# Optimization experiments

Hardware: AMD Instinct MI355X
Metric: run time of the kernel (lower is better)

## Reference

```python
import jax, jax.numpy as jnp
import numpy as np
from jax import lax

B = 4096; NLAG = 20; NT = 100; DIMH = 128; DIMPI = 2
DT = 0.01; MU1 = 0.06; MU2 = 0.02; R = 0.02; SIGMA = 0.2
BETA = 0.05; ETA = 0.5; LAMBD = 1.0; LOGEPS = 1e-6; UTIL_PENALTY = 100.0
FINAL_DISC = float(np.exp(-BETA * NT * DT))
Y_DECAY = float(np.exp(-DT * LAMBD))
# eqn.exp_array: discount weights for the lagged history (length n_lag)
EXP_ARRAY = np.exp(-LAMBD * DT * np.arange(NLAG, 0, -1)).astype(np.float32)
# eqn.geometric_sum: scalar weight on the oldest history point
GEOM = float((1.0 - np.exp(-LAMBD * DT)) / LAMBD * np.exp(-LAMBD * DT * NLAG))


def setup_inputs() -> dict:
    key = jax.random.key(0)
    ks = jax.random.split(key, 8)
    dw_sample = jax.random.normal(ks[0], (B, NT), jnp.float32) * np.sqrt(DT)
    x_init = jax.random.uniform(ks[1], (B, NLAG + 1), jnp.float32, 0.5, 1.5)
    s = 1.0 / np.sqrt(DIMH + 2)
    W_f = jax.random.normal(ks[2], (DIMH + 2, DIMH), jnp.float32) * s
    W_i = jax.random.normal(ks[3], (DIMH + 2, DIMH), jnp.float32) * s
    W_o = jax.random.normal(ks[4], (DIMH + 2, DIMH), jnp.float32) * s
    W_c = jax.random.normal(ks[5], (DIMH + 2, DIMH), jnp.float32) * s
    W_pi = jax.random.normal(ks[6], (DIMH, DIMPI), jnp.float32) * (1.0 / np.sqrt(DIMH))
    return {
        'dw_sample': dw_sample, 'x_init': x_init,
        'W_f': W_f, 'b_f': jnp.zeros((DIMH,), jnp.float32),
        'W_i': W_i, 'b_i': jnp.zeros((DIMH,), jnp.float32),
        'W_o': W_o, 'b_o': jnp.zeros((DIMH,), jnp.float32),
        'W_c': W_c, 'b_c': jnp.zeros((DIMH,), jnp.float32),
        'W_pi': W_pi, 'b_pi': jnp.zeros((DIMPI,), jnp.float32),
    }


def _forward(dw_sample, x_init, W_f, b_f, W_i, b_i, W_o, b_o, W_c, b_c, W_pi, b_pi):
    # Fuse the 4 gate Dense layers into one matmul (same math).
    W_all = jnp.concatenate([W_f, W_i, W_o, W_c], axis=1)   # [H+2, 4H]
    b_all = jnp.concatenate([b_f, b_i, b_o, b_c], axis=0)   # [4H]
    exp_arr = jnp.asarray(EXP_ARRAY)

    def cell(t_scal, x_col, h, C):
        tv = jnp.full((x_col.shape[0], 1), t_scal, x_col.dtype)
        z = jnp.concatenate([x_col, h, tv], axis=1)          # [B, H+2]
        g = z @ W_all + b_all                                # [B, 4H]
        f, i, o, cb = jnp.split(g, 4, axis=1)
        C = C * jax.nn.sigmoid(f) + jnp.tanh(cb) * jax.nn.sigmoid(i)
        h = jax.nn.sigmoid(o) * jnp.tanh(C)
        pi = h @ W_pi + b_pi                                 # [B, 2]
        return pi, h, C

    def util(v):
        return jnp.log(jax.nn.relu(v) + LOGEPS)

    # hidden_init (fixinit=False): warm up LSTM over n_lag history steps
    h0 = jnp.concatenate([x_init[:, 0:1], jnp.zeros((B, DIMH - 1), x_init.dtype)], axis=1)
    C0 = h0
    init_ts = jnp.arange(-NLAG, 0, dtype=x_init.dtype) * DT  # [NLAG]
    init_xs = x_init[:, 1:].T                                # [NLAG, B]

    def init_step(carry, inp):
        h, C = carry
        tval, xcol = inp
        _, h, C = cell(tval, xcol[:, None], h, C)
        return (h, C), None

    (h, C), _ = lax.scan(init_step, (h0, C0), (init_ts, init_xs))

    x = x_init[:, -1]
    y = jnp.sum(exp_arr * x_init[:, 1:], axis=-1) * DT + GEOM * x_init[:, 0]
    reward = jnp.zeros((B,), x.dtype)

    def step(carry, inp):
        x, y, h, C, reward = carry
        t_i, dw = inp
        t = t_i.astype(x.dtype)
        pi, h, C = cell(t * DT, x[:, None], h, C)
        pi = jax.nn.sigmoid(pi) * 2.0                        # final_pi_tf
        p0, p1 = pi[:, 0], pi[:, 1]
        inst_r = util(p0 * x) * jnp.exp(-BETA * t * DT) - jax.nn.relu(-x) * UTIL_PENALTY
        reward = reward + inst_r * DT
        dx = ((MU1 - R) * p1 - p0 + R) * x + MU2 * y
        x = x + dx * DT + SIGMA * x * p1 * dw
        y = y * Y_DECAY + x * DT
        return (x, y, h, C, reward), None

    ts = jnp.arange(NT)
    (x, y, h, C, reward), _ = lax.scan(step, (x, y, h, C, reward), (ts, dw_sample.T))

    # t == nt terminal step
    reward = reward + util(x + ETA * y) / BETA * FINAL_DISC - jax.nn.relu(-x) * UTIL_PENALTY
    return -reward


def reference(dw_sample, x_init, W_f, b_f, W_i, b_i, W_o, b_o, W_c, b_c, W_pi, b_pi):
    return _forward(dw_sample, x_init, W_f, b_f, W_i, b_i, W_o, b_o, W_c, b_c, W_pi, b_pi)
```

## Files before the change

### kernel.cpp

```cpp
#include <hip/hip_runtime.h>

#define NLAGC 20
#define NTC   100
#define DTC   0.01f
#define MU1C  0.06f
#define MU2C  0.02f
#define RC    0.02f
#define SIGC  0.2f
#define BETAC 0.05f
#define ETAC  0.5f
#define EPSC  1e-6f
#define UPENC 100.0f
#define YDECC 0.99004983374916805f
#define FDISCC 0.95122942450071403f
#define GEOMC 0.0081465072f
#define DFACTC 0.99950012497916927f

#define SPB 16
#define TPB 512
#define NKT 4
#define ZSTR 136

typedef __attribute__((ext_vector_type(8))) short short8v;
typedef __attribute__((ext_vector_type(4))) float f32x4;

__device__ __forceinline__ float sigm(float x){ return __builtin_amdgcn_rcpf(1.0f+__expf(-x)); }
__device__ __forceinline__ float tanhr(float x){ return 1.0f-2.0f*__builtin_amdgcn_rcpf(1.0f+__expf(2.0f*x)); }
__device__ __forceinline__ unsigned short f2bf(float f){
    unsigned u=__float_as_uint(f);
    u += 0x7fffu + ((u>>16)&1u);
    return (unsigned short)(u>>16);
}
__device__ __forceinline__ unsigned short f2bf_rna(float f){
    return (unsigned short)((__float_as_uint(f)+0x8000u)>>16);
}

__global__ __launch_bounds__(TPB,2) void polstm(
    const float* __restrict__ dw,  const float* __restrict__ xin,
    const float* __restrict__ Wf,  const float* __restrict__ bfp,
    const float* __restrict__ Wi,  const float* __restrict__ bip,
    const float* __restrict__ Wo,  const float* __restrict__ bop,
    const float* __restrict__ Wc,  const float* __restrict__ bcp,
    const float* __restrict__ Wpi, const float* __restrict__ bpi,
    float* __restrict__ out)
{
    __shared__ __align__(16) unsigned short zbuf[2][SPB*ZSTR];
    __shared__ float dwl[SPB*NTC];
    __shared__ float xl[SPB*21];
    __shared__ __align__(16) float pibuf[2][SPB];

    const int tid=threadIdx.x, w=tid>>6, lane=tid&63, col=lane&15, kg=lane>>4;
    const int j=w*16+col;
    const int base=blockIdx.x*SPB;

    for(int e=tid;e<2*SPB*ZSTR;e+=TPB) ((unsigned short*)zbuf)[e]=0;
    for(int e=tid;e<SPB*NTC;e+=TPB) dwl[e]=dw[base*NTC+e];
    for(int e=tid;e<SPB*21;e+=TPB)  xl[e]=xin[base*21+e];

    short8v bw[4][NKT], bpif[NKT];
    float wx[4], wt[4], bg[4];
    #pragma unroll
    for(int g=0;g<4;++g){
        const float* Wp=(g==0)?Wf:(g==1)?Wi:(g==2)?Wo:Wc;
        const float* bv=(g==0)?bfp:(g==1)?bip:(g==2)?bop:bcp;
        wx[g]=Wp[j]; wt[g]=Wp[129*128+j]; bg[g]=bv[j];
        #pragma unroll
        for(int kt=0;kt<NKT;++kt){
            short8v f;
            #pragma unroll
            for(int i=0;i<8;++i) f[i]=(short)f2bf(Wp[(1+kt*32+kg*8+i)*128+j]);
            bw[g][kt]=f;
        }
    }
    #pragma unroll
    for(int kt=0;kt<NKT;++kt){
        short8v f;
        #pragma unroll
        for(int i=0;i<8;++i){
            int k=kt*32+kg*8+i;
            int idx=k*2+((col<2)?col:0);
            float v=Wpi[idx];
            f[i]=(short)((col<2)?f2bf(v):(unsigned short)0);
        }
        bpif[kt]=f;
    }
    const float bp0=bpi[0], bp1=bpi[1];

    __syncthreads();

    float C[4];
    #pragma unroll
    for(int r=0;r<4;++r) C[r]=(j==0)?xl[(kg*4+r)*21]:0.0f;

    float xs=0.f, ys=0.f, rew=0.f;
    if(lane<SPB){
        float x0=xl[lane*21];
        xs=xl[lane*21+20];
        float acc=0.f;
        #pragma unroll
        for(int i=0;i<NLAGC;++i) acc+=__expf(-DTC*(float)(NLAGC-i))*xl[lane*21+1+i];
        ys=acc*DTC+GEOMC*x0;
    }
    if(j==0){
        #pragma unroll
        for(int r=0;r<4;++r) zbuf[0][(kg*4+r)*ZSTR+0]=f2bf(xl[(kg*4+r)*21]);
    }

    unsigned short* zr=zbuf[0];
    unsigned short* zw=zbuf[1];

    #pragma unroll 1
    for(int m=0;m<NLAGC;++m){
        __syncthreads();
        short8v av[NKT];
        {   const unsigned short* zp=zr+col*ZSTR+kg*8;
            #pragma unroll
            for(int kt=0;kt<NKT;++kt) av[kt]=*(const short8v*)(zp+kt*32);
        }
        float tval=(float)(m-NLAGC)*DTC;
        float xr0=xl[(kg*4+0)*21+1+m], xr1=xl[(kg*4+1)*21+1+m];
        float xr2=xl[(kg*4+2)*21+1+m], xr3=xl[(kg*4+3)*21+1+m];
        float b0=fmaf(wt[0],tval,bg[0]), b1=fmaf(wt[1],tval,bg[1]);
        float b2=fmaf(wt[2],tval,bg[2]), b3=fmaf(wt[3],tval,bg[3]);
        f32x4 a0={fmaf(wx[0],xr0,b0),fmaf(wx[0],xr1,b0),fmaf(wx[0],xr2,b0),fmaf(wx[0],xr3,b0)};
        f32x4 a1={fmaf(wx[1],xr0,b1),fmaf(wx[1],xr1,b1),fmaf(wx[1],xr2,b1),fmaf(wx[1],xr3,b1)};
        f32x4 a2={fmaf(wx[2],xr0,b2),fmaf(wx[2],xr1,b2),fmaf(wx[2],xr2,b2),fmaf(wx[2],xr3,b2)};
        f32x4 a3={fmaf(wx[3],xr0,b3),fmaf(wx[3],xr1,b3),fmaf(wx[3],xr2,b3),fmaf(wx[3],xr3,b3)};
        #pragma unroll
        for(int kt=0;kt<NKT;++kt){
            a0=__builtin_amdgcn_mfma_f32_16x16x32_bf16(av[kt],bw[0][kt],a0,0,0,0);
            a1=__builtin_amdgcn_mfma_f32_16x16x32_bf16(av[kt],bw[1][kt],a1,0,0,0);
            a2=__builtin_amdgcn_mfma_f32_16x16x32_bf16(av[kt],bw[2][kt],a2,0,0,0);
            a3=__builtin_amdgcn_mfma_f32_16x16x32_bf16(av[kt],bw[3][kt],a3,0,0,0);
        }
        #pragma unroll
        for(int r=0;r<4;++r){
            C[r]=C[r]*sigm(a0[r])+tanhr(a3[r])*sigm(a1[r]);
            float h=sigm(a2[r])*tanhr(C[r]);
            zw[(kg*4+r)*ZSTR+j]=f2bf_rna(h);
        }
        unsigned short* tp=zr; zr=zw; zw=tp;
    }

    float disc=1.0f;
    #pragma unroll 1
    for(int t=0;t<=NTC;++t){
        __syncthreads();
        short8v av[NKT];
        {   const unsigned short* zp=zr+col*ZSTR+kg*8;
            #pragma unroll
            for(int kt=0;kt<NKT;++kt) av[kt]=*(const short8v*)(zp+kt*32);
        }
        f32x4 a4={0.f,0.f,0.f,0.f};
        #pragma unroll
        for(int kt=0;kt<NKT;++kt)
            a4=__builtin_amdgcn_mfma_f32_16x16x32_bf16(av[kt],bpif[kt],a4,0,0,0);
        float tval=(float)t*DTC;
        float tb0=fmaf(wt[0],tval,bg[0]), tb1=fmaf(wt[1],tval,bg[1]);
        float tb2=fmaf(wt[2],tval,bg[2]), tb3=fmaf(wt[3],tval,bg[3]);
        f32x4 a0={tb0,tb0,tb0,tb0}, a1={tb1,tb1,tb1,tb1};
        f32x4 a2={tb2,tb2,tb2,tb2}, a3={tb3,tb3,tb3,tb3};
        #pragma unroll
        for(int kt=0;kt<NKT;++kt){
            a0=__builtin_amdgcn_mfma_f32_16x16x32_bf16(av[kt],bw[0][kt],a0,0,0,0);
            a1=__builtin_amdgcn_mfma_f32_16x16x32_bf16(av[kt],bw[1][kt],a1,0,0,0);
            a2=__builtin_amdgcn_mfma_f32_16x16x32_bf16(av[kt],bw[2][kt],a2,0,0,0);
            a3=__builtin_amdgcn_mfma_f32_16x16x32_bf16(av[kt],bw[3][kt],a3,0,0,0);
        }
        if(col<2) *(f32x4*)&pibuf[col][kg*4] = a4;
        if(t>0 && lane<SPB){
            float p0=2.0f*sigm(pibuf[0][lane]+bp0);
            float p1=2.0f*sigm(pibuf[1][lane]+bp1);
            float ir=__logf(fmaxf(p0*xs,0.f)+EPSC)*disc-fmaxf(-xs,0.f)*UPENC;
            rew+=ir*DTC;
            float dxv=((MU1C-RC)*p1-p0+RC)*xs+MU2C*ys;
            xs=xs+dxv*DTC+SIGC*xs*p1*dwl[lane*NTC+(t-1)];
            ys=ys*YDECC+xs*DTC;
        }
        if(t>0) disc*=DFACTC;
        if(t==NTC) break;
        int srcb=(lane>>4)<<2;
        float xr0=__shfl(xs,srcb,64),   xr1=__shfl(xs,srcb+1,64);
        float xr2=__shfl(xs,srcb+2,64), xr3=__shfl(xs,srcb+3,64);
        a0[0]=fmaf(wx[0],xr0,a0[0]); a0[1]=fmaf(wx[0],xr1,a0[1]); a0[2]=fmaf(wx[0],xr2,a0[2]); a0[3]=fmaf(wx[0],xr3,a0[3]);
        a1[0]=fmaf(wx[1],xr0,a1[0]); a1[1]=fmaf(wx[1],xr1,a1[1]); a1[2]=fmaf(wx[1],xr2,a1[2]); a1[3]=fmaf(wx[1],xr3,a1[3]);
        a2[0]=fmaf(wx[2],xr0,a2[0]); a2[1]=fmaf(wx[2],xr1,a2[1]); a2[2]=fmaf(wx[2],xr2,a2[2]); a2[3]=fmaf(wx[2],xr3,a2[3]);
        a3[0]=fmaf(wx[3],xr0,a3[0]); a3[1]=fmaf(wx[3],xr1,a3[1]); a3[2]=fmaf(wx[3],xr2,a3[2]); a3[3]=fmaf(wx[3],xr3,a3[3]);
        #pragma unroll
        for(int r=0;r<4;++r){
            C[r]=C[r]*sigm(a0[r])+tanhr(a3[r])*sigm(a1[r]);
            float h=sigm(a2[r])*tanhr(C[r]);
            zw[(kg*4+r)*ZSTR+j]=f2bf_rna(h);
        }
        unsigned short* tp=zr; zr=zw; zw=tp;
    }

    if(lane<SPB){
        rew+=__logf(fmaxf(xs+ETAC*ys,0.f)+EPSC)*(FDISCC/BETAC)-fmaxf(-xs,0.f)*UPENC;
        if(w==0) out[base+lane]=-rew;
    }
}

extern "C" void kernel_launch(void* const* d_in, const int* in_sizes, int n_in,
                              void* d_out, int out_size, void* d_ws, size_t ws_size,
                              hipStream_t stream){
    const float* dw  = (const float*)d_in[0];
    const float* xin = (const float*)d_in[1];
    const float* Wf  = (const float*)d_in[2];
    const float* bf  = (const float*)d_in[3];
    const float* Wi  = (const float*)d_in[4];
    const float* bi  = (const float*)d_in[5];
    const float* Wo  = (const float*)d_in[6];
    const float* bo  = (const float*)d_in[7];
    const float* Wc  = (const float*)d_in[8];
    const float* bc  = (const float*)d_in[9];
    const float* Wpi = (const float*)d_in[10];
    const float* bpi = (const float*)d_in[11];
    float* out = (float*)d_out;
    int nblk = (out_size + SPB - 1) / SPB;
    polstm<<<dim3(nblk), dim3(TPB), 0, stream>>>(dw, xin, Wf, bf, Wi, bi, Wo, bo, Wc, bc, Wpi, bpi, out);
}
```

Measured before the change: 150.1 us.

## Split LSTM matmul K across wave pairs and redistribute nonlinearity via LDS

Doubles the block to 1024 threads. Each pair of waves splits the 128-wide hidden reduction in half, and the partial gate sums are written to a shared gacc buffer. Each thread then combines the two halves for two hidden units of one sample, so the sigmoid/tanh work is spread over all threads instead of 16x4 per-wave accumulators. This shortens the per-step MFMA chain and nonlinearity latency on the serial recurrence, at the cost of two or three extra barriers per step, extra LDS traffic, and larger blocks with lower occupancy.

```diff
diff --git a/kernel.cpp b/kernel.cpp
--- a/kernel.cpp
+++ b/kernel.cpp
@@ -14,12 +14,10 @@
 #define YDECC 0.99004983374916805f
 #define FDISCC 0.95122942450071403f
 #define GEOMC 0.0081465072f
-#define DFACTC 0.99950012497916927f
-
-#define SPB 16
-#define TPB 512
-#define NKT 4
-#define ZSTR 136
+
+#define TPB   1024
+#define ZSTR  136
+#define GUS   132
 
 typedef __attribute__((ext_vector_type(8))) short short8v;
 typedef __attribute__((ext_vector_type(4))) float f32x4;
@@ -35,7 +33,57 @@
     return (unsigned short)((__float_as_uint(f)+0x8000u)>>16);
 }
 
-__global__ __launch_bounds__(TPB,2) void polstm(
+#define MFMA(AV,BV,AC) __builtin_amdgcn_mfma_f32_16x16x32_bf16(AV,BV,AC,0,0,0)
+
+#define P1() do{ \
+    const unsigned short* zp_=zr+col*ZSTR+half*64+kg*8; \
+    short8v av0_=*(const short8v*)(zp_); \
+    short8v av1_=*(const short8v*)(zp_+32); \
+    f32x4 z4_={0.f,0.f,0.f,0.f}; \
+    f32x4 a0_=z4_,a1_=z4_,a2_=z4_,a3_=z4_; \
+    a0_=MFMA(av0_,bw[0][0],a0_); a1_=MFMA(av0_,bw[1][0],a1_); \
+    a2_=MFMA(av0_,bw[2][0],a2_); a3_=MFMA(av0_,bw[3][0],a3_); \
+    a0_=MFMA(av1_,bw[0][1],a0_); a1_=MFMA(av1_,bw[1][1],a1_); \
+    a2_=MFMA(av1_,bw[2][1],a2_); a3_=MFMA(av1_,bw[3][1],a3_); \
+    _Pragma("unroll") \
+    for(int r_=0;r_<4;++r_){ \
+        f32x4 v_={a0_[r_],a1_[r_],a2_[r_],a3_[r_]}; \
+        *(f32x4*)&gacc[j*GUS+(kg*4+r_)*8+half*4]=v_; \
+    } \
+    if(cg==0){ \
+        f32x4 a4_=z4_; \
+        a4_=MFMA(av0_,bpif[0],a4_); \
+        a4_=MFMA(av1_,bpif[1],a4_); \
+        if(col<2) *(f32x4*)&pib[(half*2+col)*16+kg*4]=a4_; \
+    } \
+}while(0)
+
+#define COMBINE(PRE) do{ \
+    _Pragma("unroll") \
+    for(int c_=0;c_<2;++c_){ \
+        f32x4 v0_=*(const f32x4*)&gacc[(u0+c_)*GUS+s*8]; \
+        f32x4 v1_=*(const f32x4*)&gacc[(u0+c_)*GUS+s*8+4]; \
+        _Pragma("unroll") \
+        for(int g_=0;g_<4;++g_) PRE[c_][g_]=v0_[g_]+v1_[g_]; \
+    } \
+}while(0)
+
+#define NONLIN(PRE,XV,TV) do{ \
+    unsigned hp_=0; \
+    _Pragma("unroll") \
+    for(int c_=0;c_<2;++c_){ \
+        float g0_=fmaf(wx2[0][c_],(XV),fmaf(wt2[0][c_],(TV),PRE[c_][0]+bg2[0][c_])); \
+        float g1_=fmaf(wx2[1][c_],(XV),fmaf(wt2[1][c_],(TV),PRE[c_][1]+bg2[1][c_])); \
+        float g2_=fmaf(wx2[2][c_],(XV),fmaf(wt2[2][c_],(TV),PRE[c_][2]+bg2[2][c_])); \
+        float g3_=fmaf(wx2[3][c_],(XV),fmaf(wt2[3][c_],(TV),PRE[c_][3]+bg2[3][c_])); \
+        Creg[c_]=Creg[c_]*sigm(g0_)+tanhr(g3_)*sigm(g1_); \
+        float h_=sigm(g2_)*tanhr(Creg[c_]); \
+        hp_|=(unsigned)f2bf_rna(h_)<<(16*c_); \
+    } \
+    *(unsigned*)&zw[s*ZSTR+u0]=hp_; \
+}while(0)
+
+__global__ __launch_bounds__(TPB) void polstm(
     const float* __restrict__ dw,  const float* __restrict__ xin,
     const float* __restrict__ Wf,  const float* __restrict__ bfp,
     const float* __restrict__ Wi,  const float* __restrict__ bip,
@@ -44,56 +92,69 @@
     const float* __restrict__ Wpi, const float* __restrict__ bpi,
     float* __restrict__ out)
 {
-    __shared__ __align__(16) unsigned short zbuf[2][SPB*ZSTR];
-    __shared__ float dwl[SPB*NTC];
-    __shared__ float xl[SPB*21];
-    __shared__ __align__(16) float pibuf[2][SPB];
+    __shared__ __align__(16) float gacc[128*GUS];
+    __shared__ __align__(16) unsigned short zbuf[2][16*ZSTR];
+    __shared__ float dwl[16*NTC];
+    __shared__ float xl[16*21];
+    __shared__ __align__(16) float pib[2*2*16];
+    __shared__ float xcur[16];
 
     const int tid=threadIdx.x, w=tid>>6, lane=tid&63, col=lane&15, kg=lane>>4;
-    const int j=w*16+col;
-    const int base=blockIdx.x*SPB;
-
-    for(int e=tid;e<2*SPB*ZSTR;e+=TPB) ((unsigned short*)zbuf)[e]=0;
-    for(int e=tid;e<SPB*NTC;e+=TPB) dwl[e]=dw[base*NTC+e];
-    for(int e=tid;e<SPB*21;e+=TPB)  xl[e]=xin[base*21+e];
-
-    short8v bw[4][NKT], bpif[NKT];
-    float wx[4], wt[4], bg[4];
+    const int half=w&1, cg=w>>1, j=cg*16+col;
+    const int s=tid&15, u0=(tid>>4)<<1;
+    const int base=blockIdx.x*16;
+    const int wid=__builtin_amdgcn_readfirstlane(w);
+
+    for(int e=tid;e<2*16*ZSTR;e+=TPB) ((unsigned short*)zbuf)[e]=0;
+    for(int e=tid;e<16*NTC;e+=TPB) dwl[e]=dw[base*NTC+e];
+    for(int e=tid;e<16*21;e+=TPB)  xl[e]=xin[base*21+e];
+
+    short8v bw[4][2], bpif[2];
+    #pragma unroll
+    for(int g=0;g<4;++g){
+        const float* Wp=(g==0)?Wf:(g==1)?Wi:(g==2)?Wo:Wc;
+        #pragma unroll
+        for(int kt=0;kt<2;++kt){
+            short8v f;
+            #pragma unroll
+            for(int i=0;i<8;++i) f[i]=(short)f2bf(Wp[(1+half*64+kt*32+kg*8+i)*128+j]);
+            bw[g][kt]=f;
+        }
+    }
+    #pragma unroll
+    for(int kt=0;kt<2;++kt){
+        short8v f;
+        #pragma unroll
+        for(int i=0;i<8;++i){
+            int k=half*64+kt*32+kg*8+i;
+            float v=Wpi[k*2+((col<2)?col:0)];
+            f[i]=(short)((col<2)?f2bf(v):(unsigned short)0);
+        }
+        bpif[kt]=f;
+    }
+    float wx2[4][2], wt2[4][2], bg2[4][2];
     #pragma unroll
     for(int g=0;g<4;++g){
         const float* Wp=(g==0)?Wf:(g==1)?Wi:(g==2)?Wo:Wc;
         const float* bv=(g==0)?bfp:(g==1)?bip:(g==2)?bop:bcp;
-        wx[g]=Wp[j]; wt[g]=Wp[129*128+j]; bg[g]=bv[j];
-        #pragma unroll
-        for(int kt=0;kt<NKT;++kt){
-            short8v f;
-            #pragma unroll
-            for(int i=0;i<8;++i) f[i]=(short)f2bf(Wp[(1+kt*32+kg*8+i)*128+j]);
-            bw[g][kt]=f;
-        }
-    }
-    #pragma unroll
-    for(int kt=0;kt<NKT;++kt){
-        short8v f;
-        #pragma unroll
-        for(int i=0;i<8;++i){
-            int k=kt*32+kg*8+i;
-            int idx=k*2+((col<2)?col:0);
-            float v=Wpi[idx];
-            f[i]=(short)((col<2)?f2bf(v):(unsigned short)0);
-        }
-        bpif[kt]=f;
+        #pragma unroll
+        for(int c=0;c<2;++c){
+            wx2[g][c]=Wp[u0+c];
+            wt2[g][c]=Wp[129*128+u0+c];
+            bg2[g][c]=bv[u0+c];
+        }
     }
     const float bp0=bpi[0], bp1=bpi[1];
 
     __syncthreads();
 
-    float C[4];
-    #pragma unroll
-    for(int r=0;r<4;++r) C[r]=(j==0)?xl[(kg*4+r)*21]:0.0f;
+    float Creg[2];
+    Creg[0]=(u0==0)?xl[s*21]:0.0f;
+    Creg[1]=0.0f;
+    if(tid<16) zbuf[0][tid*ZSTR]=f2bf(xl[tid*21]);
 
     float xs=0.f, ys=0.f, rew=0.f;
-    if(lane<SPB){
+    if(wid==0 && lane<16){
         float x0=xl[lane*21];
         xs=xl[lane*21+20];
         float acc=0.f;
@@ -101,103 +162,74 @@
         for(int i=0;i<NLAGC;++i) acc+=__expf(-DTC*(float)(NLAGC-i))*xl[lane*21+1+i];
         ys=acc*DTC+GEOMC*x0;
     }
-    if(j==0){
-        #pragma unroll
-        for(int r=0;r<4;++r) zbuf[0][(kg*4+r)*ZSTR+0]=f2bf(xl[(kg*4+r)*21]);
-    }
-
-    unsigned short* zr=zbuf[0];
-    unsigned short* zw=zbuf[1];
+
+    unsigned short *zr=zbuf[0], *zw=zbuf[1];
 
     #pragma unroll 1
     for(int m=0;m<NLAGC;++m){
         __syncthreads();
-        short8v av[NKT];
-        {   const unsigned short* zp=zr+col*ZSTR+kg*8;
-            #pragma unroll
-            for(int kt=0;kt<NKT;++kt) av[kt]=*(const short8v*)(zp+kt*32);
-        }
-        float tval=(float)(m-NLAGC)*DTC;
-        float xr0=xl[(kg*4+0)*21+1+m], xr1=xl[(kg*4+1)*21+1+m];
-        float xr2=xl[(kg*4+2)*21+1+m], xr3=xl[(kg*4+3)*21+1+m];
-        float b0=fmaf(wt[0],tval,bg[0]), b1=fmaf(wt[1],tval,bg[1]);
-        float b2=fmaf(wt[2],tval,bg[2]), b3=fmaf(wt[3],tval,bg[3]);
-        f32x4 a0={fmaf(wx[0],xr0,b0),fmaf(wx[0],xr1,b0),fmaf(wx[0],xr2,b0),fmaf(wx[0],xr3,b0)};
-        f32x4 a1={fmaf(wx[1],xr0,b1),fmaf(wx[1],xr1,b1),fmaf(wx[1],xr2,b1),fmaf(wx[1],xr3,b1)};
-        f32x4 a2={fmaf(wx[2],xr0,b2),fmaf(wx[2],xr1,b2),fmaf(wx[2],xr2,b2),fmaf(wx[2],xr3,b2)};
-        f32x4 a3={fmaf(wx[3],xr0,b3),fmaf(wx[3],xr1,b3),fmaf(wx[3],xr2,b3),fmaf(wx[3],xr3,b3)};
-        #pragma unroll
-        for(int kt=0;kt<NKT;++kt){
-            a0=__builtin_amdgcn_mfma_f32_16x16x32_bf16(av[kt],bw[0][kt],a0,0,0,0);
-            a1=__builtin_amdgcn_mfma_f32_16x16x32_bf16(av[kt],bw[1][kt],a1,0,0,0);
-            a2=__builtin_amdgcn_mfma_f32_16x16x32_bf16(av[kt],bw[2][kt],a2,0,0,0);
-            a3=__builtin_amdgcn_mfma_f32_16x16x32_bf16(av[kt],bw[3][kt],a3,0,0,0);
-        }
-        #pragma unroll
-        for(int r=0;r<4;++r){
-            C[r]=C[r]*sigm(a0[r])+tanhr(a3[r])*sigm(a1[r]);
-            float h=sigm(a2[r])*tanhr(C[r]);
-            zw[(kg*4+r)*ZSTR+j]=f2bf_rna(h);
-        }
+        P1();
+        __syncthreads();
+        float pre[2][4];
+        COMBINE(pre);
+        float xv=xl[s*21+1+m];
+        float tv=(float)(m-NLAGC)*DTC;
+        NONLIN(pre,xv,tv);
         unsigned short* tp=zr; zr=zw; zw=tp;
     }
-
-    float disc=1.0f;
+    if(wid==0 && lane<16) xcur[lane]=xs;
+
     #pragma unroll 1
-    for(int t=0;t<=NTC;++t){
-        __syncthreads();
-        short8v av[NKT];
-        {   const unsigned short* zp=zr+col*ZSTR+kg*8;
-            #pragma unroll
-            for(int kt=0;kt<NKT;++kt) av[kt]=*(const short8v*)(zp+kt*32);
-        }
-        f32x4 a4={0.f,0.f,0.f,0.f};
-        #pragma unroll
-        for(int kt=0;kt<NKT;++kt)
-            a4=__builtin_amdgcn_mfma_f32_16x16x32_bf16(av[kt],bpif[kt],a4,0,0,0);
-        float tval=(float)t*DTC;
-        float tb0=fmaf(wt[0],tval,bg[0]), tb1=fmaf(wt[1],tval,bg[1]);
-        float tb2=fmaf(wt[2],tval,bg[2]), tb3=fmaf(wt[3],tval,bg[3]);
-        f32x4 a0={tb0,tb0,tb0,tb0}, a1={tb1,tb1,tb1,tb1};
-        f32x4 a2={tb2,tb2,tb2,tb2}, a3={tb3,tb3,tb3,tb3};
-        #pragma unroll
-        for(int kt=0;kt<NKT;++kt){
-            a0=__builtin_amdgcn_mfma_f32_16x16x32_bf16(av[kt],bw[0][kt],a0,0,0,0);
-            a1=__builtin_amdgcn_mfma_f32_16x16x32_bf16(av[kt],bw[1][kt],a1,0,0,0);
-            a2=__builtin_amdgcn_mfma_f32_16x16x32_bf16(av[kt],bw[2][kt],a2,0,0,0);
-            a3=__builtin_amdgcn_mfma_f32_16x16x32_bf16(av[kt],bw[3][kt],a3,0,0,0);
-        }
-        if(col<2) *(f32x4*)&pibuf[col][kg*4] = a4;
-        if(t>0 && lane<SPB){
-            float p0=2.0f*sigm(pibuf[0][lane]+bp0);
-            float p1=2.0f*sigm(pibuf[1][lane]+bp1);
-            float ir=__logf(fmaxf(p0*xs,0.f)+EPSC)*disc-fmaxf(-xs,0.f)*UPENC;
-            rew+=ir*DTC;
-            float dxv=((MU1C-RC)*p1-p0+RC)*xs+MU2C*ys;
-            xs=xs+dxv*DTC+SIGC*xs*p1*dwl[lane*NTC+(t-1)];
-            ys=ys*YDECC+xs*DTC;
-        }
-        if(t>0) disc*=DFACTC;
-        if(t==NTC) break;
-        int srcb=(lane>>4)<<2;
-        float xr0=__shfl(xs,srcb,64),   xr1=__shfl(xs,srcb+1,64);
-        float xr2=__shfl(xs,srcb+2,64), xr3=__shfl(xs,srcb+3,64);
-        a0[0]=fmaf(wx[0],xr0,a0[0]); a0[1]=fmaf(wx[0],xr1,a0[1]); a0[2]=fmaf(wx[0],xr2,a0[2]); a0[3]=fmaf(wx[0],xr3,a0[3]);
-        a1[0]=fmaf(wx[1],xr0,a1[0]); a1[1]=fmaf(wx[1],xr1,a1[1]); a1[2]=fmaf(wx[1],xr2,a1[2]); a1[3]=fmaf(wx[1],xr3,a1[3]);
-        a2[0]=fmaf(wx[2],xr0,a2[0]); a2[1]=fmaf(wx[2],xr1,a2[1]); a2[2]=fmaf(wx[2],xr2,a2[2]); a2[3]=fmaf(wx[2],xr3,a2[3]);
-        a3[0]=fmaf(wx[3],xr0,a3[0]); a3[1]=fmaf(wx[3],xr1,a3[1]); a3[2]=fmaf(wx[3],xr2,a3[2]); a3[3]=fmaf(wx[3],xr3,a3[3]);
-        #pragma unroll
-        for(int r=0;r<4;++r){
-            C[r]=C[r]*sigm(a0[r])+tanhr(a3[r])*sigm(a1[r]);
-            float h=sigm(a2[r])*tanhr(C[r]);
-            zw[(kg*4+r)*ZSTR+j]=f2bf_rna(h);
-        }
+    for(int t=0;t<NTC;++t){
+        __syncthreads();
+        P1();
+        __syncthreads();
+        float pre[2][4];
+        COMBINE(pre);
+        if(wid==0 && t>0){
+            if(lane<16){
+                float p0=bp0+pib[(0*2+0)*16+lane]+pib[(1*2+0)*16+lane];
+                float p1=bp1+pib[(0*2+1)*16+lane]+pib[(1*2+1)*16+lane];
+                p0=2.0f*sigm(p0);
+                p1=2.0f*sigm(p1);
+                float disc=__expf(-BETAC*(float)(t-1)*DTC);
+                rew+=(__logf(fmaxf(p0*xs,0.f)+EPSC)*disc-fmaxf(-xs,0.f)*UPENC)*DTC;
+                float dxv=((MU1C-RC)*p1-p0+RC)*xs+MU2C*ys;
+                xs=xs+dxv*DTC+SIGC*xs*p1*dwl[lane*NTC+(t-1)];
+                ys=ys*YDECC+xs*DTC;
+                xcur[lane]=xs;
+            }
+        }
+        __syncthreads();
+        float xv=xcur[s];
+        float tv=(float)t*DTC;
+        NONLIN(pre,xv,tv);
         unsigned short* tp=zr; zr=zw; zw=tp;
     }
 
-    if(lane<SPB){
+    __syncthreads();
+    if(cg==0){
+        const unsigned short* zp_=zr+col*ZSTR+half*64+kg*8;
+        short8v av0_=*(const short8v*)(zp_);
+        short8v av1_=*(const short8v*)(zp_+32);
+        f32x4 a4_={0.f,0.f,0.f,0.f};
+        a4_=MFMA(av0_,bpif[0],a4_);
+        a4_=MFMA(av1_,bpif[1],a4_);
+        if(col<2) *(f32x4*)&pib[(half*2+col)*16+kg*4]=a4_;
+    }
+    __syncthreads();
+    if(wid==0 && lane<16){
+        float p0=bp0+pib[(0*2+0)*16+lane]+pib[(1*2+0)*16+lane];
+        float p1=bp1+pib[(0*2+1)*16+lane]+pib[(1*2+1)*16+lane];
+        p0=2.0f*sigm(p0);
+        p1=2.0f*sigm(p1);
+        float disc=__expf(-BETAC*(float)(NTC-1)*DTC);
+        rew+=(__logf(fmaxf(p0*xs,0.f)+EPSC)*disc-fmaxf(-xs,0.f)*UPENC)*DTC;
+        float dxv=((MU1C-RC)*p1-p0+RC)*xs+MU2C*ys;
+        xs=xs+dxv*DTC+SIGC*xs*p1*dwl[lane*NTC+(NTC-1)];
+        ys=ys*YDECC+xs*DTC;
         rew+=__logf(fmaxf(xs+ETAC*ys,0.f)+EPSC)*(FDISCC/BETAC)-fmaxf(-xs,0.f)*UPENC;
-        if(w==0) out[base+lane]=-rew;
+        out[base+lane]=-rew;
     }
 }
 
@@ -217,6 +249,6 @@
     const float* Wpi = (const float*)d_in[10];
     const float* bpi = (const float*)d_in[11];
     float* out = (float*)d_out;
-    int nblk = (out_size + SPB - 1) / SPB;
+    int nblk = (out_size + 15) / 16;
     polstm<<<dim3(nblk), dim3(TPB), 0, stream>>>(dw, xin, Wf, bf, Wi, bi, Wo, bo, Wc, bc, Wpi, bpi, out);
 }
```

Result: slower. 195.3 us (+30.0%).
